# Performance work log

Measured on AMD Instinct MI355X. Metric: run time of the kernel, lower is better.

Reference implementation:

```python
import jax, jax.numpy as jnp
import numpy as np

T, B, F_, C, H = 500, 16, 32, 64, 64


def _gru(x, h0, w_ih, w_hh, b_ih, b_hh):
    # x: [T, N, C], h0: [N, H]; PyTorch gate order: r, z, n
    xw = x @ w_ih.T + b_ih  # [T, N, 3H] precomputed input projections

    def step(h, xw_t):
        hw = h @ w_hh.T + b_hh
        xr, xz, xn = jnp.split(xw_t, 3, axis=-1)
        hr, hz, hn = jnp.split(hw, 3, axis=-1)
        r = jax.nn.sigmoid(xr + hr)
        z = jax.nn.sigmoid(xz + hz)
        n = jnp.tanh(xn + r * hn)
        h_new = (1.0 - z) * n + z * h
        return h_new, h_new

    hT, ys = jax.lax.scan(step, h0, xw)
    return ys, hT


def setup_inputs() -> dict:
    key = jax.random.key(0)
    ks = jax.random.split(key, 16)
    s = 1.0 / np.sqrt(H)
    inp = {
        "input": jax.random.normal(ks[0], (T, B, F_, C), dtype=jnp.float32),
        "state": jnp.zeros((3, B * F_, H), dtype=jnp.float32),
    }
    i = 1
    for name in ("q", "k", "v"):
        inp[f"w_ih_{name}"] = jax.random.uniform(ks[i], (3 * H, C), jnp.float32, -s, s); i += 1
        inp[f"w_hh_{name}"] = jax.random.uniform(ks[i], (3 * H, H), jnp.float32, -s, s); i += 1
        inp[f"b_ih_{name}"] = jax.random.uniform(ks[i], (3 * H,), jnp.float32, -s, s); i += 1
        inp[f"b_hh_{name}"] = jax.random.uniform(ks[i], (3 * H,), jnp.float32, -s, s); i += 1
    inp["w_o"] = jax.random.uniform(ks[13], (C, H), jnp.float32, -s, s)
    inp["b_o"] = jax.random.uniform(ks[14], (C,), jnp.float32, -s, s)
    return inp


def reference(input, state, w_ih_q, w_hh_q, b_ih_q, b_hh_q,
              w_ih_k, w_hh_k, b_ih_k, b_hh_k,
              w_ih_v, w_hh_v, b_ih_v, b_hh_v, w_o, b_o):
    t, b, f, c = input.shape
    x = input.reshape(t, b * f, c)
    q, h_q = _gru(x, state[0], w_ih_q, w_hh_q, b_ih_q, b_hh_q)
    k, h_k = _gru(x, state[1], w_ih_k, w_hh_k, b_ih_k, b_hh_k)
    v, h_v = _gru(x, state[2], w_ih_v, w_hh_v, b_ih_v, b_hh_v)
    q = q.reshape(t, b, f, H)
    k = k.reshape(t, b, f, H)
    v = v.reshape(t, b, f, H)
    w = jnp.einsum('tbfh,tbgh->tbfg', q, k)        # q @ k^T over freq
    v = jnp.einsum('tbfg,tbgh->tbfh', w, v)        # weights @ v
    v = jax.nn.softmax(v, axis=-2)                 # softmax over freq dim
    o = v @ w_o.T + b_o                            # [t, b, f, c]
    new_state = jnp.stack([h_q, h_k, h_v], axis=0)
    return o, new_state
```

## Files before the change

kernel.cpp:

```cpp
#include <hip/hip_runtime.h>

typedef _Float16 f16x8  __attribute__((ext_vector_type(8)));
typedef float    f32x16 __attribute__((ext_vector_type(16)));

#define TSTEPS 500
#define NB 512
#define LOG2E 1.442695041f

__device__ __forceinline__ double exp_d(double v){
  v = fmin(fmax(v, -700.0), 700.0);
  double t = v * 1.4426950408889634;
  double n = rint(t);
  double f = fma(-n, 6.931471803691238e-01, v);
  f = fma(-n, 1.9082149292705877e-10, f);
  double p = 2.5052108385441718e-08;
  p = fma(p, f, 2.7557319223985893e-07);
  p = fma(p, f, 2.7557319223985888e-06);
  p = fma(p, f, 2.4801587301587302e-05);
  p = fma(p, f, 1.9841269841269841e-04);
  p = fma(p, f, 1.3888888888888889e-03);
  p = fma(p, f, 8.3333333333333332e-03);
  p = fma(p, f, 4.1666666666666664e-02);
  p = fma(p, f, 1.6666666666666666e-01);
  p = fma(p, f, 0.5);
  p = fma(p, f, 1.0);
  p = fma(p, f, 1.0);
  long long bits = (1023LL + (long long)n) << 52;
  return p * __longlong_as_double(bits);
}

__global__ __launch_bounds__(256, 2) void gru_f64(
    const float* __restrict__ x,
    const float* __restrict__ st,
    const float* __restrict__ wih0, const float* __restrict__ whh0,
    const float* __restrict__ bih0, const float* __restrict__ bhh0,
    const float* __restrict__ wih1, const float* __restrict__ whh1,
    const float* __restrict__ bih1, const float* __restrict__ bhh1,
    const float* __restrict__ wih2, const float* __restrict__ whh2,
    const float* __restrict__ bih2, const float* __restrict__ bhh2,
    _Float16* __restrict__ qkv,
    float* __restrict__ out_state)
{
  __shared__ __align__(16) double hsh[2][72];
  __shared__ __align__(16) double xsh[2][72];

  const int tid = threadIdx.x;
  const int j = tid >> 2;
  const int q = tid & 3;
  const int g = blockIdx.x >> 9;
  const int n = blockIdx.x & 511;

  const float* wih = (g==0) ? wih0 : ((g==1) ? wih1 : wih2);
  const float* whh = (g==0) ? whh0 : ((g==1) ? whh1 : whh2);
  const float* bih = (g==0) ? bih0 : ((g==1) ? bih1 : bih2);
  const float* bhh = (g==0) ? bhh0 : ((g==1) ? bhh1 : bhh2);

  double wiR[16], wiZ[16], wiN[16], whR[16], whZ[16], whN[16];
  {
    const float4* pR = (const float4*)(wih + (size_t)(       j)*64 + q*16);
    const float4* pZ = (const float4*)(wih + (size_t)( 64 + j)*64 + q*16);
    const float4* pN = (const float4*)(wih + (size_t)(128 + j)*64 + q*16);
    const float4* rR = (const float4*)(whh + (size_t)(       j)*64 + q*16);
    const float4* rZ = (const float4*)(whh + (size_t)( 64 + j)*64 + q*16);
    const float4* rN = (const float4*)(whh + (size_t)(128 + j)*64 + q*16);
    #pragma unroll
    for (int k=0;k<4;++k){
      float4 a;
      a = pR[k]; wiR[4*k]=(double)a.x; wiR[4*k+1]=(double)a.y; wiR[4*k+2]=(double)a.z; wiR[4*k+3]=(double)a.w;
      a = pZ[k]; wiZ[4*k]=(double)a.x; wiZ[4*k+1]=(double)a.y; wiZ[4*k+2]=(double)a.z; wiZ[4*k+3]=(double)a.w;
      a = pN[k]; wiN[4*k]=(double)a.x; wiN[4*k+1]=(double)a.y; wiN[4*k+2]=(double)a.z; wiN[4*k+3]=(double)a.w;
      a = rR[k]; whR[4*k]=(double)a.x; whR[4*k+1]=(double)a.y; whR[4*k+2]=(double)a.z; whR[4*k+3]=(double)a.w;
      a = rZ[k]; whZ[4*k]=(double)a.x; whZ[4*k+1]=(double)a.y; whZ[4*k+2]=(double)a.z; whZ[4*k+3]=(double)a.w;
      a = rN[k]; whN[4*k]=(double)a.x; whN[4*k+1]=(double)a.y; whN[4*k+2]=(double)a.z; whN[4*k+3]=(double)a.w;
    }
  }
  const double bRi  = (q==0) ? ((double)bih[j]    + (double)bhh[j]   ) : 0.0;
  const double bZi  = (q==0) ? ((double)bih[64+j] + (double)bhh[64+j]) : 0.0;
  const double biNi = (q==0) ? (double)bih[128+j] : 0.0;
  const double bhNi = (q==0) ? (double)bhh[128+j] : 0.0;

  double h = (double)st[(size_t)(g*512 + n)*64 + j];

  const float* xp = x + (size_t)n*64 + tid;
  float xc0 = 0.f, xc1 = 0.f;
  if (tid < 64){
    int ci = tid + 2*(tid>>4);
    hsh[0][ci] = (double)st[(size_t)(g*512 + n)*64 + tid];
    xsh[0][ci] = (double)xp[0];
    xc0 = xp[(size_t)NB*64];
    xc1 = xp[(size_t)2*NB*64];
  }
  _Float16* qout = qkv + ((size_t)g*TSTEPS*NB + n)*64 + j;
  __syncthreads();

  for (int t=0; t<TSTEPS; ++t){
    const int cur = t & 1, nxt = cur ^ 1;
    const double2* hp = (const double2*)(&hsh[cur][18*q]);
    const double2* xq = (const double2*)(&xsh[cur][18*q]);

    double hdR=bRi, hdZ=bZi, hdN=bhNi, xdR=0.0, xdZ=0.0, xdN=biNi;
    #pragma unroll
    for (int w=0; w<4; ++w){
      double2 h01 = hp[2*w], h23 = hp[2*w+1];
      double2 x01 = xq[2*w], x23 = xq[2*w+1];
      hdR = fma(whR[4*w+0], h01.x, hdR); hdR = fma(whR[4*w+1], h01.y, hdR);
      hdR = fma(whR[4*w+2], h23.x, hdR); hdR = fma(whR[4*w+3], h23.y, hdR);
      hdZ = fma(whZ[4*w+0], h01.x, hdZ); hdZ = fma(whZ[4*w+1], h01.y, hdZ);
      hdZ = fma(whZ[4*w+2], h23.x, hdZ); hdZ = fma(whZ[4*w+3], h23.y, hdZ);
      hdN = fma(whN[4*w+0], h01.x, hdN); hdN = fma(whN[4*w+1], h01.y, hdN);
      hdN = fma(whN[4*w+2], h23.x, hdN); hdN = fma(whN[4*w+3], h23.y, hdN);
      xdR = fma(wiR[4*w+0], x01.x, xdR); xdR = fma(wiR[4*w+1], x01.y, xdR);
      xdR = fma(wiR[4*w+2], x23.x, xdR); xdR = fma(wiR[4*w+3], x23.y, xdR);
      xdZ = fma(wiZ[4*w+0], x01.x, xdZ); xdZ = fma(wiZ[4*w+1], x01.y, xdZ);
      xdZ = fma(wiZ[4*w+2], x23.x, xdZ); xdZ = fma(wiZ[4*w+3], x23.y, xdZ);
      xdN = fma(wiN[4*w+0], x01.x, xdN); xdN = fma(wiN[4*w+1], x01.y, xdN);
      xdN = fma(wiN[4*w+2], x23.x, xdN); xdN = fma(wiN[4*w+3], x23.y, xdN);
    }
    hdR += __shfl_xor(hdR, 1, 64); hdR += __shfl_xor(hdR, 2, 64);
    hdZ += __shfl_xor(hdZ, 1, 64); hdZ += __shfl_xor(hdZ, 2, 64);
    hdN += __shfl_xor(hdN, 1, 64); hdN += __shfl_xor(hdN, 2, 64);
    xdR += __shfl_xor(xdR, 1, 64); xdR += __shfl_xor(xdR, 2, 64);
    xdZ += __shfl_xor(xdZ, 1, 64); xdZ += __shfl_xor(xdZ, 2, 64);
    xdN += __shfl_xor(xdN, 1, 64); xdN += __shfl_xor(xdN, 2, 64);

    double r  = 1.0/(1.0 + exp_d(-(xdR + hdR)));
    double z  = 1.0/(1.0 + exp_d(-(xdZ + hdZ)));
    double yn = xdN + r*hdN;
    double nn = 1.0 - 2.0/(exp_d(2.0*yn) + 1.0);
    h = (1.0 - z)*nn + z*h;

    if (q == 0){
      hsh[nxt][j + 2*(j>>4)] = h;
      qout[(size_t)t*NB*64] = (_Float16)(float)h;
    }
    if (tid < 64){
      xsh[nxt][tid + 2*(tid>>4)] = (double)xc0;
      int tp = (t+3 < TSTEPS) ? (t+3) : (TSTEPS-1);
      float xnx = xp[(size_t)tp*NB*64];
      xc0 = xc1; xc1 = xnx;
    }
    __syncthreads();
  }

  if (q == 0)
    out_state[(size_t)(g*512 + n)*64 + j] = (float)h;
}

__global__ __launch_bounds__(64) void attn(
    const _Float16* __restrict__ qkv,
    const float* __restrict__ w_o,
    const float* __restrict__ b_o,
    float* __restrict__ out)
{
  __shared__ __align__(16) _Float16 Qs[32*72];
  __shared__ __align__(16) _Float16 Ks[32*72];
  __shared__ __align__(16) _Float16 Vt[64*40];
  __shared__ __align__(16) _Float16 Wm[32*40];
  __shared__ __align__(16) _Float16 wols[64*72];
  __shared__ float bo[64];

  const int lane = threadIdx.x;
  const int t = blockIdx.x >> 4;
  const int b = blockIdx.x & 15;
  const size_t base    = ((size_t)t*NB + b*32)*64;
  const size_t gstride = (size_t)TSTEPS*NB*64;

  #pragma unroll
  for (int it=0; it<4; ++it){
    int idx = it*64 + lane;
    int f = idx >> 3, ko = (idx & 7)*8;
    *(f16x8*)&Qs[f*72+ko] = *(const f16x8*)&qkv[base + (size_t)f*64 + ko];
    *(f16x8*)&Ks[f*72+ko] = *(const f16x8*)&qkv[gstride + base + (size_t)f*64 + ko];
  }
  #pragma unroll
  for (int it=0; it<32; ++it){
    int idx = it*64 + lane;
    int f = idx >> 6, hh = idx & 63;
    Vt[hh*40 + f] = qkv[2*gstride + base + (size_t)f*64 + hh];
  }
  #pragma unroll
  for (int it=0; it<32; ++it){
    int idx = it*64 + lane;
    int c = idx >> 5, hp = (idx & 31)*2;
    float2 u = *(const float2*)(w_o + c*64 + hp);
    wols[c*72 + hp]     = (_Float16)u.x;
    wols[c*72 + hp + 1] = (_Float16)u.y;
  }
  bo[lane] = b_o[lane];

  const int m  = lane & 31;
  const int hk = (lane >> 5) * 8;
  const int rbase = (lane >> 5) * 4;

  f32x16 accW;
  #pragma unroll
  for (int i=0;i<16;++i) accW[i]=0.f;
  #pragma unroll
  for (int kb=0; kb<4; ++kb){
    f16x8 a  = *(const f16x8*)&Qs[m*72 + kb*16 + hk];
    f16x8 bb = *(const f16x8*)&Ks[m*72 + kb*16 + hk];
    accW = __builtin_amdgcn_mfma_f32_32x32x16_f16(a, bb, accW, 0, 0, 0);
  }
  #pragma unroll
  for (int r=0; r<16; ++r){
    int row = (r&3) + 8*(r>>2) + rbase;
    Wm[row*40 + m] = (_Float16)accW[r];
  }

  f32x16 accA0, accA1;
  #pragma unroll
  for (int i=0;i<16;++i){ accA0[i]=0.f; accA1[i]=0.f; }
  #pragma unroll
  for (int kb=0; kb<2; ++kb){
    f16x8 a  = *(const f16x8*)&Wm[m*40 + kb*16 + hk];
    f16x8 b0 = *(const f16x8*)&Vt[(     m)*40 + kb*16 + hk];
    f16x8 b1 = *(const f16x8*)&Vt[(32 + m)*40 + kb*16 + hk];
    accA0 = __builtin_amdgcn_mfma_f32_32x32x16_f16(a, b0, accA0, 0, 0, 0);
    accA1 = __builtin_amdgcn_mfma_f32_32x32x16_f16(a, b1, accA1, 0, 0, 0);
  }

  float mx0 = accA0[0], mx1 = accA1[0];
  #pragma unroll
  for (int r=1;r<16;++r){ mx0 = fmaxf(mx0, accA0[r]); mx1 = fmaxf(mx1, accA1[r]); }
  mx0 = fmaxf(mx0, __shfl_xor(mx0, 32, 64));
  mx1 = fmaxf(mx1, __shfl_xor(mx1, 32, 64));
  float s0 = 0.f, s1 = 0.f;
  #pragma unroll
  for (int r=0;r<16;++r){
    float e0 = __builtin_amdgcn_exp2f(LOG2E*(accA0[r]-mx0)); accA0[r]=e0; s0+=e0;
    float e1 = __builtin_amdgcn_exp2f(LOG2E*(accA1[r]-mx1)); accA1[r]=e1; s1+=e1;
  }
  s0 += __shfl_xor(s0, 32, 64);
  s1 += __shfl_xor(s1, 32, 64);
  float i0 = __builtin_amdgcn_rcpf(s0), i1 = __builtin_amdgcn_rcpf(s1);
  #pragma unroll
  for (int r=0;r<16;++r){
    int row = (r&3) + 8*(r>>2) + rbase;
    Qs[row*72 + m]      = (_Float16)(accA0[r]*i0);
    Qs[row*72 + 32 + m] = (_Float16)(accA1[r]*i1);
  }

  f32x16 accO0, accO1;
  #pragma unroll
  for (int i=0;i<16;++i){ accO0[i]=0.f; accO1[i]=0.f; }
  #pragma unroll
  for (int kb=0; kb<4; ++kb){
    f16x8 a  = *(const f16x8*)&Qs[m*72 + kb*16 + hk];
    f16x8 b0 = *(const f16x8*)&wols[(     m)*72 + kb*16 + hk];
    f16x8 b1 = *(const f16x8*)&wols[(32 + m)*72 + kb*16 + hk];
    accO0 = __builtin_amdgcn_mfma_f32_32x32x16_f16(a, b0, accO0, 0, 0, 0);
    accO1 = __builtin_amdgcn_mfma_f32_32x32x16_f16(a, b1, accO1, 0, 0, 0);
  }
  const size_t obase = ((size_t)t*16 + b)*2048;
  #pragma unroll
  for (int r=0;r<16;++r){
    int row = (r&3) + 8*(r>>2) + rbase;
    out[obase + row*64 + m]      = accO0[r] + bo[m];
    out[obase + row*64 + 32 + m] = accO1[r] + bo[32+m];
  }
}

extern "C" void kernel_launch(void* const* d_in, const int* in_sizes, int n_in,
                              void* d_out, int out_size, void* d_ws, size_t ws_size,
                              hipStream_t stream)
{
  const float* x  = (const float*)d_in[0];
  const float* st = (const float*)d_in[1];
  _Float16* qkv = (_Float16*)d_ws;
  float* out = (float*)d_out;
  float* out_state = out + (size_t)16384000;

  gru_f64<<<dim3(1536), dim3(256), 0, stream>>>(
    x, st,
    (const float*)d_in[2],  (const float*)d_in[3],
    (const float*)d_in[4],  (const float*)d_in[5],
    (const float*)d_in[6],  (const float*)d_in[7],
    (const float*)d_in[8],  (const float*)d_in[9],
    (const float*)d_in[10], (const float*)d_in[11],
    (const float*)d_in[12], (const float*)d_in[13],
    qkv, out_state);

  attn<<<dim3(8000), dim3(64), 0, stream>>>(
    qkv, (const float*)d_in[14], (const float*)d_in[15], out);
}
```

Before: 2.253 ms.

## Compute GRU gate nonlinearities once per unit in one wave; use fast f64 reciprocal

Before, all four lanes of each hidden unit redundantly ran the f64 exp and divide gate math. Now the reduced gate pre-activations go to shared memory, one wavefront does the nonlinearity and state update, and a second wavefront handles the x prefetch. The f64 divisions become v_rcp_f64 plus two Newton steps, and the hidden/x buffers drop from double to single buffering. This cuts redundant f64 ALU work, at the cost of an extra __syncthreads and an extra shared-memory round trip on every serial timestep.

```diff
diff --git a/kernel.cpp b/kernel.cpp
--- a/kernel.cpp
+++ b/kernel.cpp
@@ -29,6 +29,14 @@
   return p * __longlong_as_double(bits);
 }
 
+__device__ __forceinline__ double rcp_nr(double x){
+  double r;
+  asm("v_rcp_f64 %0, %1" : "=v"(r) : "v"(x));
+  r = fma(fma(-x, r, 1.0), r, r);
+  r = fma(fma(-x, r, 1.0), r, r);
+  return r;
+}
+
 __global__ __launch_bounds__(256, 2) void gru_f64(
     const float* __restrict__ x,
     const float* __restrict__ st,
@@ -41,8 +49,9 @@
     _Float16* __restrict__ qkv,
     float* __restrict__ out_state)
 {
-  __shared__ __align__(16) double hsh[2][72];
-  __shared__ __align__(16) double xsh[2][72];
+  __shared__ __align__(16) double hsh[72];
+  __shared__ __align__(16) double xsh[72];
+  __shared__ __align__(16) double psh[4][72];
 
   const int tid = threadIdx.x;
   const int j = tid >> 2;
@@ -79,24 +88,25 @@
   const double biNi = (q==0) ? (double)bih[128+j] : 0.0;
   const double bhNi = (q==0) ? (double)bhh[128+j] : 0.0;
 
-  double h = (double)st[(size_t)(g*512 + n)*64 + j];
-
-  const float* xp = x + (size_t)n*64 + tid;
+  const int l2 = tid & 63;
+  const float* xp = x + (size_t)n*64 + l2;
+
+  double h = 0.0;
   float xc0 = 0.f, xc1 = 0.f;
   if (tid < 64){
-    int ci = tid + 2*(tid>>4);
-    hsh[0][ci] = (double)st[(size_t)(g*512 + n)*64 + tid];
-    xsh[0][ci] = (double)xp[0];
+    h = (double)st[(size_t)(g*512 + n)*64 + tid];
+    hsh[tid + 2*(tid>>4)] = h;
+  } else if (tid < 128){
+    xsh[l2 + 2*(l2>>4)] = (double)xp[0];
     xc0 = xp[(size_t)NB*64];
     xc1 = xp[(size_t)2*NB*64];
   }
-  _Float16* qout = qkv + ((size_t)g*TSTEPS*NB + n)*64 + j;
+  _Float16* qout = qkv + ((size_t)g*TSTEPS*NB + n)*64 + tid;
   __syncthreads();
 
   for (int t=0; t<TSTEPS; ++t){
-    const int cur = t & 1, nxt = cur ^ 1;
-    const double2* hp = (const double2*)(&hsh[cur][18*q]);
-    const double2* xq = (const double2*)(&xsh[cur][18*q]);
+    const double2* hp = (const double2*)(&hsh[18*q]);
+    const double2* xq = (const double2*)(&xsh[18*q]);
 
     double hdR=bRi, hdZ=bZi, hdN=bhNi, xdR=0.0, xdZ=0.0, xdN=biNi;
     #pragma unroll
@@ -123,18 +133,28 @@
     xdZ += __shfl_xor(xdZ, 1, 64); xdZ += __shfl_xor(xdZ, 2, 64);
     xdN += __shfl_xor(xdN, 1, 64); xdN += __shfl_xor(xdN, 2, 64);
 
-    double r  = 1.0/(1.0 + exp_d(-(xdR + hdR)));
-    double z  = 1.0/(1.0 + exp_d(-(xdZ + hdZ)));
-    double yn = xdN + r*hdN;
-    double nn = 1.0 - 2.0/(exp_d(2.0*yn) + 1.0);
-    h = (1.0 - z)*nn + z*h;
-
     if (q == 0){
-      hsh[nxt][j + 2*(j>>4)] = h;
+      psh[0][j] = hdR + xdR;
+      psh[1][j] = hdZ + xdZ;
+      psh[2][j] = xdN;
+      psh[3][j] = hdN;
+    }
+    __syncthreads();
+
+    if (tid < 64){
+      double aR = psh[0][tid];
+      double aZ = psh[1][tid];
+      double xn = psh[2][tid];
+      double hn = psh[3][tid];
+      double r  = rcp_nr(1.0 + exp_d(-aR));
+      double z  = rcp_nr(1.0 + exp_d(-aZ));
+      double yn = xn + r*hn;
+      double nn = 1.0 - 2.0*rcp_nr(exp_d(2.0*yn) + 1.0);
+      h = (1.0 - z)*nn + z*h;
+      hsh[tid + 2*(tid>>4)] = h;
       qout[(size_t)t*NB*64] = (_Float16)(float)h;
-    }
-    if (tid < 64){
-      xsh[nxt][tid + 2*(tid>>4)] = (double)xc0;
+    } else if (tid < 128){
+      xsh[l2 + 2*(l2>>4)] = (double)xc0;
       int tp = (t+3 < TSTEPS) ? (t+3) : (TSTEPS-1);
       float xnx = xp[(size_t)tp*NB*64];
       xc0 = xc1; xc1 = xnx;
@@ -142,8 +162,8 @@
     __syncthreads();
   }
 
-  if (q == 0)
-    out_state[(size_t)(g*512 + n)*64 + j] = (float)h;
+  if (tid < 64)
+    out_state[(size_t)(g*512 + n)*64 + tid] = (float)h;
 }
 
 __global__ __launch_bounds__(64) void attn(
```

Result: faster. 2.177 ms (-3.3%).
